# Performance work log

Measured on AMD Instinct MI355X. Metric: run time of the kernel, lower is better.

The kernel has to match this reference:

```python
import jax, jax.numpy as jnp
import numpy as np

B, N, T, F, NC = 4, 16, 2048, 512, 43
EPS = 1e-5


def setup_inputs() -> dict:
    key = jax.random.key(0)
    ks = jax.random.split(key, 8)
    bbox = jax.random.normal(ks[0], (B, N, 4, T), jnp.float32)
    bbox_class = jax.random.randint(ks[1], (B, N, T), 0, NC, jnp.int32)
    edge_map = jax.random.uniform(ks[2], (B, N, N, T), jnp.float32)
    W_lin = jax.random.normal(ks[3], (F, 4), jnp.float32) * 0.1          # nn.Linear(4, F) weight [F,4]
    emb_table = jax.random.normal(ks[4], (NC, F), jnp.float32) * 0.1
    emb_table = emb_table.at[0].set(0.0)                                  # padding_idx=0
    W1 = jax.random.normal(ks[5], (F, 2 * F), jnp.float32) * (1.0 / np.sqrt(2 * F))  # 1x1 conv2d [F,2F]
    W2 = jax.random.normal(ks[6], (F, F), jnp.float32) * (1.0 / np.sqrt(F))          # 1x1 conv2d [F,F]
    Wm = jax.random.normal(ks[7], (F, F, N), jnp.float32) * (1.0 / np.sqrt(F * N))   # conv1d merge [F,F,N]
    ln_w = jnp.ones((F,), jnp.float32)
    ln_b = jnp.zeros((F,), jnp.float32)
    return {"bbox": bbox, "bbox_class": bbox_class, "edge_map": edge_map,
            "W_lin": W_lin, "emb_table": emb_table, "W1": W1, "W2": W2,
            "Wm": Wm, "ln_w": ln_w, "ln_b": ln_b}


def reference(bbox, bbox_class, edge_map, W_lin, emb_table, W1, W2, Wm, ln_w, ln_b):
    # edge_map [B,N,N,T] -> [B,T,N,N]
    em = jnp.transpose(edge_map, (0, 3, 1, 2))
    # class embedding: [B,N,T] -> [B,T,N] -> [B,T,N,F]
    cls_e = emb_table[jnp.transpose(bbox_class, (0, 2, 1))]
    # bbox linear: [B,N,4,T] x [F,4] -> [B,T,N,F]
    box_e = jnp.einsum('bnct,fc->btnf', bbox, W_lin)
    # cat along features: note original concatenates (class_embed, bbox_embed)
    node = jnp.concatenate([cls_e, box_e], axis=-1)        # [B,T,N,2F]
    node = jnp.einsum('btnc,fc->btnf', node, W1)           # 1x1 conv
    node = jax.nn.relu(jnp.einsum('btij,btjf->btif', em, node))
    node = jnp.einsum('btnc,fc->btnf', node, W2)           # 1x1 conv
    node = jax.nn.relu(jnp.einsum('btij,btjf->btif', em, node))
    # conv1d over node axis with kernel size N collapses N: [B,T,F]
    feat = jnp.einsum('btnc,fcn->btf', node, Wm)
    # LayerNorm over channel dim of [B,F,T]
    x = jnp.transpose(feat, (0, 2, 1))                     # [B,F,T]
    mu = jnp.mean(x, axis=1, keepdims=True)
    r = x - mu
    var = jnp.mean(r * r, axis=1, keepdims=True)
    out = r / jnp.sqrt(var + EPS)
    return out * ln_w[None, :, None] + ln_b[None, :, None]
```

## Files before the change

### kernel.cpp

```cpp
#include <hip/hip_runtime.h>
#include <hip/hip_bf16.h>

#define B_  4
#define N_  16
#define T_  2048
#define F_  512
#define NC_ 43
constexpr float LN_EPS = 1e-5f;

constexpr int EMB1_N = NC_ * F_;
constexpr int WBOX_N = F_ * 4;
constexpr int W2BF_N = F_ * F_;
constexpr int WMT_N  = F_ * N_ * F_;
constexpr int K_TOT  = N_ * F_;

typedef __bf16 bf16x8_t __attribute__((ext_vector_type(8)));
typedef float  f32x4_t  __attribute__((ext_vector_type(4)));

__device__ __forceinline__ void gload16(const void* g, void* l) {
  __builtin_amdgcn_global_load_lds(
      (const __attribute__((address_space(1))) unsigned int*)g,
      (__attribute__((address_space(3))) unsigned int*)l, 16, 0, 0);
}

__device__ __forceinline__ short bf16s(float x) {
  return (short)__bfloat16_as_ushort(__float2bfloat16(x));
}
__device__ __forceinline__ unsigned bf16u(float x) {
  return (unsigned)__bfloat16_as_ushort(__float2bfloat16(x));
}

__global__ __launch_bounds__(256) void precompute_small(
    const float* __restrict__ emb_table, const float* __restrict__ W1,
    const float* __restrict__ W_lin, const float* __restrict__ W2,
    float* __restrict__ emb1, float* __restrict__ wbox,
    __hip_bfloat16* __restrict__ w2bf)
{
  int idx = blockIdx.x * 256 + threadIdx.x;
  if (idx < EMB1_N) {
    int k = idx >> 9, f = idx & 511;
    const float4* et = (const float4*)&emb_table[k * F_];
    const float4* w1 = (const float4*)&W1[f * (2 * F_)];
    float s = 0.f;
    for (int c4 = 0; c4 < F_ / 4; ++c4) {
      float4 a = et[c4], b = w1[c4];
      s = fmaf(a.x, b.x, s); s = fmaf(a.y, b.y, s);
      s = fmaf(a.z, b.z, s); s = fmaf(a.w, b.w, s);
    }
    emb1[idx] = s;
  } else if (idx < EMB1_N + WBOX_N) {
    int t2 = idx - EMB1_N;
    int f = t2 >> 2, q = t2 & 3;
    const float4* w1 = (const float4*)&W1[f * (2 * F_) + F_];
    float s = 0.f;
    for (int c4 = 0; c4 < F_ / 4; ++c4) {
      float4 a = w1[c4];
      s = fmaf(a.x, W_lin[(c4 * 4 + 0) * 4 + q], s);
      s = fmaf(a.y, W_lin[(c4 * 4 + 1) * 4 + q], s);
      s = fmaf(a.z, W_lin[(c4 * 4 + 2) * 4 + q], s);
      s = fmaf(a.w, W_lin[(c4 * 4 + 3) * 4 + q], s);
    }
    wbox[t2] = s;
  } else if (idx < EMB1_N + WBOX_N + W2BF_N) {
    int t3 = idx - (EMB1_N + WBOX_N);
    w2bf[t3] = __float2bfloat16(W2[t3]);
  }
}

__global__ __launch_bounds__(256) void precompute_wmT(
    const float* __restrict__ Wm, __hip_bfloat16* __restrict__ wmT)
{
  __shared__ float tile[16 * 517];
  const int f = blockIdx.x;
  const float* src = Wm + (long long)f * 8192;
  for (int i = threadIdx.x; i < 8192; i += 256) {
    int c = i >> 4, n = i & 15;
    tile[n * 517 + c] = src[i];
  }
  __syncthreads();
  short* dst = (short*)wmT + (long long)f * 8192;
  for (int i = threadIdx.x; i < 4096; i += 256) {
    int o = i << 1;
    int n = o >> 9, c = o & 511;
    short2 sv;
    sv.x = bf16s(tile[n * 517 + c]);
    sv.y = bf16s(tile[n * 517 + c + 1]);
    *(short2*)&dst[o] = sv;
  }
}

#define N1ST 20
__global__ __launch_bounds__(256) void k_h1g(
    const float* __restrict__ bbox, const int* __restrict__ cls,
    const float* __restrict__ edge, const float* __restrict__ emb1,
    const float* __restrict__ wbox, __hip_bfloat16* __restrict__ g)
{
  __shared__ __align__(16) short em_bf[256];
  __shared__ __align__(16) short n1T[F_ * N1ST + 32];
  __shared__ int   cls_s[N_];
  __shared__ float bb_s[N_ * 4];

  const int p = blockIdx.x;
  const int b = p >> 11;
  const int t = p & 2047;
  const int tid = threadIdx.x;

  {
    int i = tid >> 4, j = tid & 15;
    em_bf[tid] = bf16s(edge[(((b * N_ + i) * N_ + j) * T_) + t]);
  }
  if (tid < N_) cls_s[tid] = cls[(b * N_ + tid) * T_ + t];
  if (tid < N_ * 4) {
    int j = tid >> 2, qq = tid & 3;
    bb_s[tid] = bbox[(((b * N_ + j) * 4 + qq) * T_) + t];
  }
  __syncthreads();

  const float4* wb4 = (const float4*)wbox;
  for (int idx = tid; idx < N_ * F_ / 4; idx += 256) {
    int j = idx >> 7, f4 = idx & 127;
    float4 e = *(const float4*)&emb1[cls_s[j] * F_ + f4 * 4];
    float b0 = bb_s[j * 4 + 0], b1 = bb_s[j * 4 + 1];
    float b2 = bb_s[j * 4 + 2], b3 = bb_s[j * 4 + 3];
    float4 w0 = wb4[f4 * 4 + 0], w1 = wb4[f4 * 4 + 1];
    float4 w2 = wb4[f4 * 4 + 2], w3 = wb4[f4 * 4 + 3];
    int f = f4 * 4;
    float v0 = e.x; v0 = fmaf(b0, w0.x, v0); v0 = fmaf(b1, w0.y, v0);
    v0 = fmaf(b2, w0.z, v0); v0 = fmaf(b3, w0.w, v0);
    float v1 = e.y; v1 = fmaf(b0, w1.x, v1); v1 = fmaf(b1, w1.y, v1);
    v1 = fmaf(b2, w1.z, v1); v1 = fmaf(b3, w1.w, v1);
    float v2 = e.z; v2 = fmaf(b0, w2.x, v2); v2 = fmaf(b1, w2.y, v2);
    v2 = fmaf(b2, w2.z, v2); v2 = fmaf(b3, w2.w, v2);
    float v3 = e.w; v3 = fmaf(b0, w3.x, v3); v3 = fmaf(b1, w3.y, v3);
    v3 = fmaf(b2, w3.z, v3); v3 = fmaf(b3, w3.w, v3);
    n1T[(f + 0) * N1ST + j] = bf16s(v0);
    n1T[(f + 1) * N1ST + j] = bf16s(v1);
    n1T[(f + 2) * N1ST + j] = bf16s(v2);
    n1T[(f + 3) * N1ST + j] = bf16s(v3);
  }
  __syncthreads();

  const int lane = tid & 63, wv = tid >> 6;
  const int c = lane & 15;
  const int q = lane >> 4;

  union { bf16x8_t v; short4 s[2]; } ef;
  ef.s[0] = (short4){0, 0, 0, 0};
  ef.s[1] = (short4){0, 0, 0, 0};
  if (q < 2) {
    ef.s[0] = *(const short4*)&em_bf[c * 16 + 8 * q];
    ef.s[1] = *(const short4*)&em_bf[c * 16 + 8 * q + 4];
  }
  const int ko = (q < 2) ? 8 * q : 0;
  const int a0 = ((32 * q + c) & 63) * 4;
  const int a1 = ((32 * q + 16 + c) & 63) * 4;

  short* gs = (short*)g;
  const long long gbase = (long long)p * (N_ * F_);

#pragma unroll
  for (int tl = 0; tl < 8; ++tl) {
    const int ft = wv * 8 + tl;
    const int row = (ft * 16 + c) * N1ST;

    union { bf16x8_t v; short4 s[2]; } bf_;
    bf_.s[0] = *(const short4*)&n1T[row + ko];
    bf_.s[1] = *(const short4*)&n1T[row + ko + 4];
    f32x4_t d1 = __builtin_amdgcn_mfma_f32_16x16x32_bf16(
        ef.v, bf_.v, (f32x4_t){0.f, 0.f, 0.f, 0.f}, 0, 0, 0);

    int pk0 = (int)((bf16u(fmaxf(d1[1], 0.f)) << 16) | bf16u(fmaxf(d1[0], 0.f)));
    int pk1 = (int)((bf16u(fmaxf(d1[3], 0.f)) << 16) | bf16u(fmaxf(d1[2], 0.f)));

    union { bf16x8_t v; int u[4]; } af_;
    af_.u[0] = __builtin_amdgcn_ds_bpermute(a0, pk0);
    af_.u[1] = __builtin_amdgcn_ds_bpermute(a0, pk1);
    af_.u[2] = __builtin_amdgcn_ds_bpermute(a1, pk0);
    af_.u[3] = __builtin_amdgcn_ds_bpermute(a1, pk1);

    f32x4_t d2 = __builtin_amdgcn_mfma_f32_16x16x32_bf16(
        af_.v, ef.v, (f32x4_t){0.f, 0.f, 0.f, 0.f}, 0, 0, 0);
    short4 gv;
    gv.x = bf16s(d2[0]);
    gv.y = bf16s(d2[1]);
    gv.z = bf16s(d2[2]);
    gv.w = bf16s(d2[3]);
    *(short4*)&gs[gbase + c * F_ + ft * 16 + 4 * q] = gv;
  }
}

__device__ __forceinline__ void stage_h2(const short* gs, const short* ws,
                                         long long m0, int kc,
                                         short* As, short* Bs,
                                         int rowU, int chkU) {
  gload16(gs + (m0 + rowU) * F_ + kc + chkU, As + rowU * 32 + chkU);
#pragma unroll
  for (int it = 0; it < 4; ++it)
    gload16(ws + (it * 128 + rowU) * F_ + kc + chkU,
            Bs + (it * 128 + rowU) * 32 + chkU);
}

__global__ __launch_bounds__(512, 2) void gemm_h2(
    __hip_bfloat16* __restrict__ gbuf, const __hip_bfloat16* __restrict__ w2bf)
{
  __shared__ __align__(16) short As[2][128 * 32];
  __shared__ __align__(16) short Bs[2][512 * 32];

  short* gs = (short*)gbuf;
  const short* ws = (const short*)w2bf;

  const int tid = threadIdx.x;
  const long long m0 = (long long)blockIdx.x * 128;
  const int wave8 = tid >> 6, lane = tid & 63;
  const int wr = wave8 >> 2, wcol = wave8 & 3;
  const int rowU = tid >> 2, chkU = (tid & 3) * 8;
  const int mrow = lane & 15, kq = (lane >> 4) * 8;

  f32x4_t acc[4][8];
#pragma unroll
  for (int i = 0; i < 4; ++i)
#pragma unroll
    for (int j = 0; j < 8; ++j) acc[i][j] = (f32x4_t){0.f, 0.f, 0.f, 0.f};

  auto compute = [&](const short* Ap, const short* Bp) {
    bf16x8_t af[4], bfr[8];
#pragma unroll
    for (int i = 0; i < 4; ++i)
      af[i] = *(const bf16x8_t*)&Ap[((wr << 6) + i * 16 + mrow) * 32 + kq];
#pragma unroll
    for (int j = 0; j < 8; ++j)
      bfr[j] = *(const bf16x8_t*)&Bp[((wcol << 7) + j * 16 + mrow) * 32 + kq];
    __builtin_amdgcn_s_setprio(1);
#pragma unroll
    for (int i = 0; i < 4; ++i)
#pragma unroll
      for (int j = 0; j < 8; ++j)
        acc[i][j] = __builtin_amdgcn_mfma_f32_16x16x32_bf16(af[i], bfr[j], acc[i][j], 0, 0, 0);
    __builtin_amdgcn_s_setprio(0);
  };

  stage_h2(gs, ws, m0, 0,  As[0], Bs[0], rowU, chkU);
  stage_h2(gs, ws, m0, 32, As[1], Bs[1], rowU, chkU);

  for (int t = 0; t < 14; ++t) {
    asm volatile("s_waitcnt vmcnt(5)" ::: "memory");
    __builtin_amdgcn_sched_barrier(0);
    __builtin_amdgcn_s_barrier();
    __builtin_amdgcn_sched_barrier(0);

    compute(As[t & 1], Bs[t & 1]);

    __builtin_amdgcn_sched_barrier(0);
    __builtin_amdgcn_s_barrier();
    __builtin_amdgcn_sched_barrier(0);
    stage_h2(gs, ws, m0, (t + 2) * 32, As[t & 1], Bs[t & 1], rowU, chkU);
  }
  asm volatile("s_waitcnt vmcnt(5)" ::: "memory");
  __builtin_amdgcn_sched_barrier(0);
  __builtin_amdgcn_s_barrier();
  __builtin_amdgcn_sched_barrier(0);
  compute(As[0], Bs[0]);
  asm volatile("s_waitcnt vmcnt(0)" ::: "memory");
  __builtin_amdgcn_sched_barrier(0);
  __builtin_amdgcn_s_barrier();
  __builtin_amdgcn_sched_barrier(0);
  compute(As[1], Bs[1]);

  const int rbase = (lane >> 4) << 2;
#pragma unroll
  for (int i = 0; i < 4; ++i)
#pragma unroll
    for (int j = 0; j < 8; ++j)
#pragma unroll
      for (int r = 0; r < 4; ++r) {
        int row = (wr << 6) + i * 16 + rbase + r;
        int col = (wcol << 7) + j * 16 + mrow;
        float v = fmaxf(acc[i][j][r], 0.f);
        gs[(m0 + row) * F_ + col] = bf16s(v);
      }
}

__global__ __launch_bounds__(512, 2) void gemm_feat(
    const __hip_bfloat16* __restrict__ h2g, const __hip_bfloat16* __restrict__ wmTg,
    float* __restrict__ out)
{
  __shared__ __align__(16) char smem[49152];
  float* sM = (float*)smem;
  float* sT = (float*)smem;

  const short* h2s  = (const short*)h2g;
  const short* wmTs = (const short*)wmTg;

  const int tid = threadIdx.x;
  const int bx = blockIdx.x;
  const int mt = bx & 127, nt = bx >> 7;
  const long long m0 = (long long)mt * 64;
  const int n0 = nt * 128;

  const int wave8 = tid >> 6;
  const int half = wave8 >> 2;
  const int wave = wave8 & 3;
  const int lane = tid & 63;
  const int wr = wave >> 1, wc = wave & 1;
  const int mrow = lane & 15;
  const int kq = (lane >> 4) * 8;

  const short* aBase = h2s + m0 * K_TOT;
  const short* bBase = wmTs + (long long)n0 * K_TOT;

  const int rowB = tid >> 2, chkB = (tid & 3) * 8;
  const int hA = tid >> 8;
  const int rA = (tid & 255) >> 2;
  const int kA = (tid & 3) * 8;

  f32x4_t acc[2][4];
#pragma unroll
  for (int i = 0; i < 2; ++i)
#pragma unroll
    for (int j = 0; j < 4; ++j) acc[i][j] = (f32x4_t){0.f, 0.f, 0.f, 0.f};

  for (int ks = 0; ks < 4096; ks += 64) {
#pragma unroll
    for (int s = 0; s < 2; ++s)
      gload16(aBase + (long long)rA * K_TOT + hA * 4096 + ks + s * 32 + kA,
              (short*)(smem + hA * 8192 + s * 4096) + rA * 32 + kA);
#pragma unroll
    for (int h = 0; h < 2; ++h)
#pragma unroll
      for (int s = 0; s < 2; ++s)
        gload16(bBase + (long long)rowB * K_TOT + h * 4096 + ks + s * 32 + chkB,
                (short*)(smem + 16384 + (h * 2 + s) * 8192) + rowB * 32 + chkB);
    __syncthreads();

#pragma unroll
    for (int s = 0; s < 2; ++s) {
      const short* AsH = (const short*)(smem + half * 8192 + s * 4096);
      const short* BsH = (const short*)(smem + 16384 + (half * 2 + s) * 8192);
      bf16x8_t af[2], bfr[4];
#pragma unroll
      for (int i = 0; i < 2; ++i)
        af[i] = *(const bf16x8_t*)&AsH[((wr << 5) + i * 16 + mrow) * 32 + kq];
#pragma unroll
      for (int j = 0; j < 4; ++j)
        bfr[j] = *(const bf16x8_t*)&BsH[((wc << 6) + j * 16 + mrow) * 32 + kq];
#pragma unroll
      for (int i = 0; i < 2; ++i)
#pragma unroll
        for (int j = 0; j < 4; ++j)
          acc[i][j] = __builtin_amdgcn_mfma_f32_16x16x32_bf16(af[i], bfr[j], acc[i][j], 0, 0, 0);
    }
    __syncthreads();
  }

  const int rq = (lane >> 4) << 2;
#pragma unroll
  for (int r = 0; r < 2; ++r) {
    if (half == 1 && wr == r) {
#pragma unroll
      for (int i = 0; i < 2; ++i)
#pragma unroll
        for (int j = 0; j < 4; ++j)
#pragma unroll
          for (int rr = 0; rr < 4; ++rr)
            sM[(i * 16 + rq + rr) * 132 + (wc << 6) + j * 16 + mrow] = acc[i][j][rr];
    }
    __syncthreads();
    if (half == 0 && wr == r) {
#pragma unroll
      for (int i = 0; i < 2; ++i)
#pragma unroll
        for (int j = 0; j < 4; ++j)
#pragma unroll
          for (int rr = 0; rr < 4; ++rr)
            acc[i][j][rr] += sM[(i * 16 + rq + rr) * 132 + (wc << 6) + j * 16 + mrow];
    }
    __syncthreads();
  }

  const int b = (int)(m0 >> 11);
  const int t0 = (int)(m0 & 2047);
#pragma unroll
  for (int cch = 0; cch < 2; ++cch) {
    if (half == 0 && wc == cch) {
#pragma unroll
      for (int i = 0; i < 2; ++i)
#pragma unroll
        for (int j = 0; j < 4; ++j)
#pragma unroll
          for (int rr = 0; rr < 4; ++rr)
            sT[((wr << 5) + i * 16 + rq + rr) * 65 + j * 16 + mrow] = acc[i][j][rr];
    }
    __syncthreads();
    long long ob = (long long)b * (F_ * T_) + (long long)(n0 + cch * 64) * T_ + t0;
    for (int idx = tid; idx < 64 * 64; idx += 512) {
      int f = idx >> 6, m = idx & 63;
      out[ob + (long long)f * T_ + m] = sT[m * 65 + f];
    }
    __syncthreads();
  }
}

__global__ __launch_bounds__(256) void ln_inplace(
    float* __restrict__ out, const float* __restrict__ lnw, const float* __restrict__ lnb)
{
  __shared__ float sF[F_ * 17];
  __shared__ float red[512];
  __shared__ float smu[16], srstd[16];

  const int tid = threadIdx.x;
  const int p0 = blockIdx.x << 4;
  const int b = p0 >> 11, t0 = p0 & 2047;
  long long ob = (long long)b * (F_ * T_) + t0;

  for (int idx = tid; idx < F_ * 16; idx += 256) {
    int f = idx >> 4, m = idx & 15;
    sF[f * 17 + m] = out[ob + (long long)f * T_ + m];
  }
  __syncthreads();

  {
    int m = tid & 15, s = tid >> 4;
    float sum = 0.f, sq = 0.f;
    for (int f = s; f < F_; f += 16) {
      float v = sF[f * 17 + m];
      sum += v; sq += v * v;
    }
    red[tid] = sum;
    red[256 + tid] = sq;
  }
  __syncthreads();
  if (tid < 16) {
    float sum = 0.f, sq = 0.f;
#pragma unroll
    for (int s = 0; s < 16; ++s) { sum += red[s * 16 + tid]; sq += red[256 + s * 16 + tid]; }
    float mu = sum * (1.f / F_);
    float var = sq * (1.f / F_) - mu * mu;
    smu[tid] = mu;
    srstd[tid] = rsqrtf(var + LN_EPS);
  }
  __syncthreads();

  for (int idx = tid; idx < F_ * 16; idx += 256) {
    int f = idx >> 4, m = idx & 15;
    float v = (sF[f * 17 + m] - smu[m]) * srstd[m] * lnw[f] + lnb[f];
    out[ob + (long long)f * T_ + m] = v;
  }
}

extern "C" void kernel_launch(void* const* d_in, const int* in_sizes, int n_in,
                              void* d_out, int out_size, void* d_ws, size_t ws_size,
                              hipStream_t stream)
{
  const float* bbox      = (const float*)d_in[0];
  const int*   cls       = (const int*)d_in[1];
  const float* edge      = (const float*)d_in[2];
  const float* W_lin     = (const float*)d_in[3];
  const float* emb_table = (const float*)d_in[4];
  const float* W1        = (const float*)d_in[5];
  const float* W2        = (const float*)d_in[6];
  const float* Wm        = (const float*)d_in[7];
  const float* lnw       = (const float*)d_in[8];
  const float* lnb       = (const float*)d_in[9];
  float* out = (float*)d_out;

  float* emb1 = (float*)d_ws;
  float* wbox = emb1 + EMB1_N;
  __hip_bfloat16* w2bf = (__hip_bfloat16*)(wbox + WBOX_N);
  __hip_bfloat16* wmT  = w2bf + W2BF_N;
  __hip_bfloat16* gbuf = wmT + WMT_N;

  precompute_small<<<(EMB1_N + WBOX_N + W2BF_N) / 256, 256, 0, stream>>>(
      emb_table, W1, W_lin, W2, emb1, wbox, w2bf);
  precompute_wmT<<<F_, 256, 0, stream>>>(Wm, wmT);
  k_h1g<<<B_ * T_, 256, 0, stream>>>(bbox, cls, edge, emb1, wbox, gbuf);
  gemm_h2<<<B_ * T_ * N_ / 128, 512, 0, stream>>>(gbuf, w2bf);
  gemm_feat<<<512, 512, 0, stream>>>(gbuf, wmT, out);
  ln_inplace<<<B_ * T_ / 16, 256, 0, stream>>>(out, lnw, lnb);
}
```

Measured before the change: 416.9 us.

## Split h2 GEMM into N-halves with triple-buffered out-of-place output

Adds a new h2 GEMM kernel that writes to a separate workspace buffer instead of in place. This lets each block compute a 128x256 tile over 2048 blocks instead of 128x512 over 1024, with a swizzled block-to-tile mapping so the two N-halves of an M tile run close together. It uses a 3-stage LDS pipeline with smaller accumulators, aiming for more parallelism and better latency hiding. The cost is that each A tile is loaded twice, more workspace is needed, and the kernel falls back to the old in-place path if the workspace is too small.

```diff
diff --git a/kernel.cpp b/kernel.cpp
--- a/kernel.cpp
+++ b/kernel.cpp
@@ -13,6 +13,7 @@
 constexpr int W2BF_N = F_ * F_;
 constexpr int WMT_N  = F_ * N_ * F_;
 constexpr int K_TOT  = N_ * F_;
+constexpr long long GBUF_N = (long long)B_ * T_ * N_ * F_;
 
 typedef __bf16 bf16x8_t __attribute__((ext_vector_type(8)));
 typedef float  f32x4_t  __attribute__((ext_vector_type(4)));
@@ -189,7 +190,113 @@
   }
 }
 
-__device__ __forceinline__ void stage_h2(const short* gs, const short* ws,
+__device__ __forceinline__ void stage_d3(const short* gs, const short* ws,
+                                         long long m0, int n0, int kc,
+                                         short* As, short* Bs,
+                                         int rowU, int chkU) {
+  gload16(gs + (m0 + rowU) * F_ + kc + chkU, As + rowU * 32 + chkU);
+#pragma unroll
+  for (int it = 0; it < 2; ++it)
+    gload16(ws + (n0 + it * 128 + rowU) * F_ + kc + chkU,
+            Bs + (it * 128 + rowU) * 32 + chkU);
+}
+
+__global__ __launch_bounds__(512, 2) void gemm_h2_d3(
+    const __hip_bfloat16* __restrict__ gbuf,
+    const __hip_bfloat16* __restrict__ w2bf,
+    __hip_bfloat16* __restrict__ h2out)
+{
+  __shared__ __align__(16) short As[3][128 * 32];
+  __shared__ __align__(16) short Bs[3][256 * 32];
+
+  const short* gs = (const short*)gbuf;
+  const short* ws = (const short*)w2bf;
+  short* hs = (short*)h2out;
+
+  const int tid = threadIdx.x;
+  const int bx = blockIdx.x;
+  const int mt = (bx & 7) | ((bx >> 4) << 3);
+  const int nt = (bx >> 3) & 1;
+  const long long m0 = (long long)mt * 128;
+  const int n0 = nt * 256;
+
+  const int wave8 = tid >> 6, lane = tid & 63;
+  const int wr = wave8 >> 2, wcol = wave8 & 3;
+  const int rowU = tid >> 2, chkU = (tid & 3) * 8;
+  const int mrow = lane & 15, kq = (lane >> 4) * 8;
+
+  f32x4_t acc[4][4];
+#pragma unroll
+  for (int i = 0; i < 4; ++i)
+#pragma unroll
+    for (int j = 0; j < 4; ++j) acc[i][j] = (f32x4_t){0.f, 0.f, 0.f, 0.f};
+
+  auto compute = [&](const short* Ap, const short* Bp) {
+    bf16x8_t af[4], bfr[4];
+#pragma unroll
+    for (int i = 0; i < 4; ++i)
+      af[i] = *(const bf16x8_t*)&Ap[((wr << 6) + i * 16 + mrow) * 32 + kq];
+#pragma unroll
+    for (int j = 0; j < 4; ++j)
+      bfr[j] = *(const bf16x8_t*)&Bp[((wcol << 6) + j * 16 + mrow) * 32 + kq];
+    __builtin_amdgcn_s_setprio(1);
+#pragma unroll
+    for (int i = 0; i < 4; ++i)
+#pragma unroll
+      for (int j = 0; j < 4; ++j)
+        acc[i][j] = __builtin_amdgcn_mfma_f32_16x16x32_bf16(af[i], bfr[j], acc[i][j], 0, 0, 0);
+    __builtin_amdgcn_s_setprio(0);
+  };
+
+  stage_d3(gs, ws, m0, n0, 0,  As[0], Bs[0], rowU, chkU);
+  stage_d3(gs, ws, m0, n0, 32, As[1], Bs[1], rowU, chkU);
+  stage_d3(gs, ws, m0, n0, 64, As[2], Bs[2], rowU, chkU);
+
+  for (int t = 0; t < 13; ++t) {
+    asm volatile("s_waitcnt vmcnt(6)" ::: "memory");
+    __builtin_amdgcn_sched_barrier(0);
+    __builtin_amdgcn_s_barrier();
+    __builtin_amdgcn_sched_barrier(0);
+
+    const int s = t % 3;
+    compute(As[s], Bs[s]);
+
+    __builtin_amdgcn_sched_barrier(0);
+    __builtin_amdgcn_s_barrier();
+    __builtin_amdgcn_sched_barrier(0);
+    stage_d3(gs, ws, m0, n0, (t + 3) * 32, As[s], Bs[s], rowU, chkU);
+  }
+  asm volatile("s_waitcnt vmcnt(6)" ::: "memory");
+  __builtin_amdgcn_sched_barrier(0);
+  __builtin_amdgcn_s_barrier();
+  __builtin_amdgcn_sched_barrier(0);
+  compute(As[1], Bs[1]);
+  asm volatile("s_waitcnt vmcnt(3)" ::: "memory");
+  __builtin_amdgcn_sched_barrier(0);
+  __builtin_amdgcn_s_barrier();
+  __builtin_amdgcn_sched_barrier(0);
+  compute(As[2], Bs[2]);
+  asm volatile("s_waitcnt vmcnt(0)" ::: "memory");
+  __builtin_amdgcn_sched_barrier(0);
+  __builtin_amdgcn_s_barrier();
+  __builtin_amdgcn_sched_barrier(0);
+  compute(As[0], Bs[0]);
+
+  const int rbase = (lane >> 4) << 2;
+#pragma unroll
+  for (int i = 0; i < 4; ++i)
+#pragma unroll
+    for (int j = 0; j < 4; ++j)
+#pragma unroll
+      for (int r = 0; r < 4; ++r) {
+        int row = (wr << 6) + i * 16 + rbase + r;
+        int col = n0 + (wcol << 6) + j * 16 + mrow;
+        float v = fmaxf(acc[i][j][r], 0.f);
+        hs[(m0 + row) * F_ + col] = bf16s(v);
+      }
+}
+
+__device__ __forceinline__ void stage_ip(const short* gs, const short* ws,
                                          long long m0, int kc,
                                          short* As, short* Bs,
                                          int rowU, int chkU) {
@@ -200,7 +307,7 @@
             Bs + (it * 128 + rowU) * 32 + chkU);
 }
 
-__global__ __launch_bounds__(512, 2) void gemm_h2(
+__global__ __launch_bounds__(512, 2) void gemm_h2_ip(
     __hip_bfloat16* __restrict__ gbuf, const __hip_bfloat16* __restrict__ w2bf)
 {
   __shared__ __align__(16) short As[2][128 * 32];
@@ -239,8 +346,8 @@
     __builtin_amdgcn_s_setprio(0);
   };
 
-  stage_h2(gs, ws, m0, 0,  As[0], Bs[0], rowU, chkU);
-  stage_h2(gs, ws, m0, 32, As[1], Bs[1], rowU, chkU);
+  stage_ip(gs, ws, m0, 0,  As[0], Bs[0], rowU, chkU);
+  stage_ip(gs, ws, m0, 32, As[1], Bs[1], rowU, chkU);
 
   for (int t = 0; t < 14; ++t) {
     asm volatile("s_waitcnt vmcnt(5)" ::: "memory");
@@ -253,7 +360,7 @@
     __builtin_amdgcn_sched_barrier(0);
     __builtin_amdgcn_s_barrier();
     __builtin_amdgcn_sched_barrier(0);
-    stage_h2(gs, ws, m0, (t + 2) * 32, As[t & 1], Bs[t & 1], rowU, chkU);
+    stage_ip(gs, ws, m0, (t + 2) * 32, As[t & 1], Bs[t & 1], rowU, chkU);
   }
   asm volatile("s_waitcnt vmcnt(5)" ::: "memory");
   __builtin_amdgcn_sched_barrier(0);
@@ -469,11 +576,22 @@
   __hip_bfloat16* wmT  = w2bf + W2BF_N;
   __hip_bfloat16* gbuf = wmT + WMT_N;
 
+  const size_t base_bytes =
+      (size_t)(EMB1_N + WBOX_N) * 4 + (size_t)(W2BF_N + WMT_N) * 2;
+  const size_t need2 = base_bytes + 2ULL * (size_t)GBUF_N * 2;
+
   precompute_small<<<(EMB1_N + WBOX_N + W2BF_N) / 256, 256, 0, stream>>>(
       emb_table, W1, W_lin, W2, emb1, wbox, w2bf);
   precompute_wmT<<<F_, 256, 0, stream>>>(Wm, wmT);
   k_h1g<<<B_ * T_, 256, 0, stream>>>(bbox, cls, edge, emb1, wbox, gbuf);
-  gemm_h2<<<B_ * T_ * N_ / 128, 512, 0, stream>>>(gbuf, w2bf);
-  gemm_feat<<<512, 512, 0, stream>>>(gbuf, wmT, out);
+
+  if (ws_size >= need2) {
+    __hip_bfloat16* h2buf = gbuf + GBUF_N;
+    gemm_h2_d3<<<2048, 512, 0, stream>>>(gbuf, w2bf, h2buf);
+    gemm_feat<<<512, 512, 0, stream>>>(h2buf, wmT, out);
+  } else {
+    gemm_h2_ip<<<1024, 512, 0, stream>>>(gbuf, w2bf);
+    gemm_feat<<<512, 512, 0, stream>>>(gbuf, wmT, out);
+  }
   ln_inplace<<<B_ * T_ / 16, 256, 0, stream>>>(out, lnw, lnb);
 }
```

Result: no change. 418.7 us (+0.4%).
